# Performance work log

Measured on AMD Instinct MI355X. Metric: run time of the kernel, lower is better.

The kernel has to match this reference:

```python
import jax, jax.numpy as jnp
import numpy as np

D_MODEL = 1024
NUM_HEAD = 16
D_HEAD = 64


def setup_inputs() -> dict:
    key = jax.random.key(0)
    ks = jax.random.split(key, 9)
    b, p = 8, 1024
    s = 1.0 / np.sqrt(D_MODEL)
    inp = {
        "x": jax.random.normal(ks[0], (b, p, D_MODEL), jnp.float32),
        "w_q": jax.random.uniform(ks[1], (D_MODEL, D_MODEL), jnp.float32, -s, s),
        "b_q": jax.random.uniform(ks[2], (D_MODEL,), jnp.float32, -s, s),
        "w_k": jax.random.uniform(ks[3], (D_MODEL, D_MODEL), jnp.float32, -s, s),
        "b_k": jax.random.uniform(ks[4], (D_MODEL,), jnp.float32, -s, s),
        "w_v": jax.random.uniform(ks[5], (D_MODEL, D_MODEL), jnp.float32, -s, s),
        "b_v": jax.random.uniform(ks[6], (D_MODEL,), jnp.float32, -s, s),
        "w_o": jax.random.uniform(ks[7], (D_MODEL, D_MODEL), jnp.float32, -s, s),
        "b_o": jax.random.uniform(ks[8], (D_MODEL,), jnp.float32, -s, s),
    }
    return inp


def reference(x, w_q, b_q, w_k, b_k, w_v, b_v, w_o, b_o):
    b, p, _ = x.shape
    # projections (torch Linear: y = x @ W.T + b; here weights stored [in,out])
    q = x @ w_q + b_q
    k = x @ w_k + b_k
    v = x @ w_v + b_v
    # [b, h, p, d]
    q = q.reshape(b, p, NUM_HEAD, D_HEAD).transpose(0, 2, 1, 3)
    k = k.reshape(b, p, NUM_HEAD, D_HEAD).transpose(0, 2, 1, 3)
    v = v.reshape(b, p, NUM_HEAD, D_HEAD).transpose(0, 2, 1, 3)
    scale = 1.0 / np.sqrt(D_HEAD).astype(np.float32)
    scores = jnp.einsum("bhqd,bhkd->bhqk", q, k) * scale
    attn = jax.nn.softmax(scores, axis=-1)
    out = jnp.einsum("bhqk,bhkd->bhqd", attn, v)
    out = out.transpose(0, 2, 1, 3).reshape(b, p, D_MODEL)
    return out @ w_o + b_o
```

## Files before the change

kernel.cpp:

```cpp
#include <hip/hip_runtime.h>
#include <stdint.h>


typedef __attribute__((ext_vector_type(8))) short short8;
typedef __attribute__((ext_vector_type(4))) short s16x4;
typedef __attribute__((ext_vector_type(4))) float f32x4;

__device__ __forceinline__ short f2bf(float f) {
  unsigned u = __builtin_bit_cast(unsigned, f);
  u += 0x7fffu + ((u >> 16) & 1u);
  return (short)(u >> 16);
}

__device__ __forceinline__ unsigned pk2bf(float a, float b) {
  unsigned ua = __builtin_bit_cast(unsigned, a);
  unsigned ub = __builtin_bit_cast(unsigned, b);
  ua += 0x7fffu + ((ua >> 16) & 1u);
  ub += 0x7fffu + ((ub >> 16) & 1u);
  return (ua >> 16) | (ub & 0xffff0000u);
}

__device__ __forceinline__ unsigned cvtpk(float a, float b) {
  unsigned r;
  asm("v_cvt_pk_bf16_f32 %0, %1, %2" : "=v"(r) : "v"(a), "v"(b));
  return r;
}

__device__ __forceinline__ float fexp2(float x) {
  float r;
  asm("v_exp_f32 %0, %1" : "=v"(r) : "v"(x));
  return r;
}

typedef __attribute__((address_space(3))) void lds_void;
typedef __attribute__((address_space(1))) void gbl_void;
#define GLD16(gp, lp) \
  __builtin_amdgcn_global_load_lds((gbl_void*)(gp), (lds_void*)(lp), 16, 0, 0)

#define MFMA(a, b, c) __builtin_amdgcn_mfma_f32_16x16x32_bf16((a), (b), (c), 0, 0, 0)

__global__ __launch_bounds__(256) void k_prep(const float* __restrict__ x,
                                              short* __restrict__ xb,
                                              const float* __restrict__ s0,
                                              const float* __restrict__ s1,
                                              const float* __restrict__ s2,
                                              const float* __restrict__ s3,
                                              short* __restrict__ d0,
                                              short* __restrict__ d1,
                                              short* __restrict__ d2,
                                              short* __restrict__ d3) {
  if (blockIdx.z == 4) {
    int t = threadIdx.y * 32 + threadIdx.x;
    int bid = blockIdx.y * 32 + blockIdx.x;
#pragma unroll
    for (int j = 0; j < 4; ++j) {
      int i = (bid * 1024 + j * 256 + t) * 8;
      const float4* s = (const float4*)(x + i);
      float4 f0 = s[0], f1 = s[1];
      short8 o;
      o[0] = f2bf(f0.x); o[1] = f2bf(f0.y); o[2] = f2bf(f0.z); o[3] = f2bf(f0.w);
      o[4] = f2bf(f1.x); o[5] = f2bf(f1.y); o[6] = f2bf(f1.z); o[7] = f2bf(f1.w);
      *(short8*)(xb + i) = o;
    }
    return;
  }
  __shared__ float tile[32][33];
  const float* srcs[4] = {s0, s1, s2, s3};
  short* dsts[4] = {d0, d1, d2, d3};
  const float* src = srcs[blockIdx.z];
  short* dst = dsts[blockIdx.z];
  int tx = threadIdx.x, ty = threadIdx.y;
  int x0 = blockIdx.x * 32, y0 = blockIdx.y * 32;
#pragma unroll
  for (int i = 0; i < 32; i += 8)
    tile[ty + i][tx] = src[(y0 + ty + i) * 1024 + x0 + tx];
  __syncthreads();
#pragma unroll
  for (int i = 0; i < 32; i += 8)
    dst[(x0 + ty + i) * 1024 + y0 + tx] = f2bf(tile[tx][ty + i]);
}

__global__ __launch_bounds__(512, 2) void k_gemm_qkv(const short* __restrict__ A,
                                                     const short* __restrict__ Bt,
                                                     const float* __restrict__ bias0,
                                                     const float* __restrict__ bias1,
                                                     const float* __restrict__ bias2,
                                                     short* __restrict__ o0,
                                                     short* __restrict__ o1,
                                                     short* __restrict__ o2) {
  __shared__ __align__(16) short a_lds[4][256 * 32];
  __shared__ __align__(16) short b_lds[4][256 * 32];
  const int tid = threadIdx.x;
  const int l = blockIdx.x;
  const int li = l >> 3;
  const int m0 = ((l & 7) * 4 + (li & 3)) << 8;
  const int n0 = (li >> 2) << 8;

  const int lane = tid & 63;
  const int ll = lane & 15;
  const int qd = lane >> 4;
  const int wm = (tid >> 8) * 128;
  const int wn = ((tid >> 6) & 3) * 64;

  const int srow = tid >> 2;
  const int gc = (tid & 3) ^ ((srow >> 1) & 3);
  const short* ag = A + (long)(m0 + srow) * 1024 + gc * 8;
  const short* bg = Bt + (long)(n0 + srow) * 1024 + gc * 8;

  const int xsl = (qd ^ ((ll >> 1) & 3)) * 8;

  f32x4 acc[8][4] = {};

#define STAGE(t)                                              \
  {                                                           \
    const int _b = (t) & 3;                                   \
    const int _k = (t) * 32;                                  \
    GLD16(ag + _k, &a_lds[_b][tid * 8]);                      \
    GLD16(ag + 131072 + _k, &a_lds[_b][4096 + tid * 8]);      \
    GLD16(bg + _k, &b_lds[_b][tid * 8]);                      \
    GLD16(bg + 131072 + _k, &b_lds[_b][4096 + tid * 8]);      \
  }

#define TILE(kt, VM, PF)                                                     \
  {                                                                          \
    asm volatile("s_waitcnt vmcnt(" #VM ")" ::: "memory");                   \
    __builtin_amdgcn_s_barrier();                                            \
    if (PF) STAGE((kt) + 3);                                                 \
    short8 af[8], bf8[4];                                                    \
    _Pragma("unroll")                                                        \
    for (int mi = 0; mi < 8; ++mi)                                           \
      af[mi] = *(const short8*)&a_lds[(kt) & 3][(wm + mi * 16 + ll) * 32 + xsl]; \
    _Pragma("unroll")                                                        \
    for (int ni = 0; ni < 4; ++ni)                                           \
      bf8[ni] = *(const short8*)&b_lds[(kt) & 3][(wn + ni * 16 + ll) * 32 + xsl]; \
    __builtin_amdgcn_s_setprio(1);                                           \
    _Pragma("unroll")                                                        \
    for (int mi = 0; mi < 8; ++mi)                                           \
      _Pragma("unroll")                                                      \
      for (int ni = 0; ni < 4; ++ni)                                         \
        acc[mi][ni] = MFMA(af[mi], bf8[ni], acc[mi][ni]);                    \
    __builtin_amdgcn_s_setprio(0);                                           \
  }

  STAGE(0); STAGE(1); STAGE(2);

#pragma unroll 4
  for (int kt = 0; kt < 28; ++kt) TILE(kt, 8, 1)
  TILE(28, 8, 1)
  TILE(29, 8, 0)
  TILE(30, 4, 0)
  TILE(31, 0, 0)

#undef TILE
#undef STAGE

  const int which = n0 >> 10;
  const int nb = n0 & 1023;
  if (which == 2) {
    const int b = m0 >> 10;
    const int p0 = (m0 & 1023) + wm;
#pragma unroll
    for (int ni = 0; ni < 4; ++ni) {
      int nl = nb + wn + ni * 16 + ll;
      float bv = bias2[nl];
      int h = nl >> 6, d = nl & 63;
#pragma unroll
      for (int mi = 0; mi < 8; ++mi) {
        int p = p0 + mi * 16 + qd * 4;
        int2 pk;
        pk.x = (int)pk2bf(acc[mi][ni][0] + bv, acc[mi][ni][1] + bv);
        pk.y = (int)pk2bf(acc[mi][ni][2] + bv, acc[mi][ni][3] + bv);
        *(int2*)&o2[(long)(b * 16 + h) * 65536 + d * 1024 + p] = pk;
      }
    }
  } else {
    const float* bias = which ? bias1 : bias0;
    short* o = which ? o1 : o0;
    const float sc = which ? 1.0f : 0.18033688f;
#pragma unroll
    for (int ni = 0; ni < 4; ++ni) {
      int nl = nb + wn + ni * 16 + ll;
      float bv = bias[nl];
      int h = nl >> 6, d = nl & 63;
#pragma unroll
      for (int mi = 0; mi < 8; ++mi)
#pragma unroll
        for (int r = 0; r < 4; ++r) {
          int m = m0 + wm + mi * 16 + qd * 4 + r;
          int b = m >> 10, p = m & 1023;
          o[(long)(b * 16 + h) * 65536 + p * 64 + d] = f2bf((acc[mi][ni][r] + bv) * sc);
        }
    }
  }
}

template <int MODE>
__global__ __launch_bounds__(256, 3) void k_gemm(const short* __restrict__ A,
                                                 const short* __restrict__ Bt,
                                                 const float* __restrict__ bias0,
                                                 const float* __restrict__ bias1,
                                                 const float* __restrict__ bias2,
                                                 short* __restrict__ o0,
                                                 short* __restrict__ o1,
                                                 short* __restrict__ o2,
                                                 float* __restrict__ of) {
  __shared__ __align__(16) short a_lds[128 * 64];
  __shared__ __align__(16) short b_lds[128 * 64];
  const int tid = threadIdx.x;
  const int l = blockIdx.x;
  const int m0 = ((((l & 7) << 3) | ((l >> 3) & 7))) << 7;
  const int n0 = (l >> 6) << 7;
  const int w = tid >> 6;
  const int lane = tid & 63;
  const int ll = lane & 15;
  const int qd = lane >> 4;
  const int wm = (w & 1) * 64;
  const int wn = (w >> 1) * 64;

  const int srow = tid >> 3;
  const int schunk = ((tid & 7) ^ (srow & 7)) * 8;
  const short* ag = A + (long)(m0 + srow) * 1024 + schunk;
  const short* bg = Bt + (long)(n0 + srow) * 1024 + schunk;

  f32x4 acc[4][4] = {};

  for (int kt = 0; kt < 1024; kt += 64) {
#pragma unroll
    for (int j = 0; j < 4; ++j) {
      GLD16(ag + j * 32768 + kt, &a_lds[j * 2048 + tid * 8]);
      GLD16(bg + j * 32768 + kt, &b_lds[j * 2048 + tid * 8]);
    }
    __syncthreads();
#pragma unroll
    for (int kh = 0; kh < 2; ++kh) {
      const int xoff = (((kh * 4 + qd) ^ (ll & 7)) * 8);
      short8 af[4], bfr[4];
#pragma unroll
      for (int mt = 0; mt < 4; ++mt)
        af[mt] = *(const short8*)&a_lds[(wm + mt * 16 + ll) * 64 + xoff];
#pragma unroll
      for (int nt = 0; nt < 4; ++nt)
        bfr[nt] = *(const short8*)&b_lds[(wn + nt * 16 + ll) * 64 + xoff];
#pragma unroll
      for (int mt = 0; mt < 4; ++mt)
#pragma unroll
        for (int nt = 0; nt < 4; ++nt)
          acc[mt][nt] = MFMA(af[mt], bfr[nt], acc[mt][nt]);
    }
    __syncthreads();
  }

  if (MODE == 0) {
  } else {
#pragma unroll
    for (int nt = 0; nt < 4; ++nt) {
      int n = n0 + wn + nt * 16 + ll;
      float bv = bias0[n];
#pragma unroll
      for (int mt = 0; mt < 4; ++mt) {
#pragma unroll
        for (int r = 0; r < 4; ++r) {
          int m = m0 + wm + mt * 16 + qd * 4 + r;
          of[(long)m * 1024 + n] = acc[mt][nt][r] + bv;
        }
      }
    }
  }
}

__global__ __launch_bounds__(256, 4) void k_attn(const short* __restrict__ Q,
                                                 const short* __restrict__ K,
                                                 const short* __restrict__ VT,
                                                 short* __restrict__ O) {
  __shared__ __align__(16) short k_lds[2][4096];
  __shared__ __align__(16) short vt_lds[2][4096];
  const int tid = threadIdx.x;
  const int w = tid >> 6, lane = tid & 63, ll = lane & 15, qd = lane >> 4;
  const int bid = blockIdx.x;
  const int xcd = bid & 7;
  const int inner = bid >> 3;
  const int bh = xcd * 16 + (inner & 15);
  const int qb = inner >> 4;
  const long hoff = (long)bh * 65536;
  const int qr0 = qb * 128 + w * 32;

  const short* qg = Q + hoff + (long)(qr0 + ll) * 64 + qd * 8;
  short8 qf[2][2];
  qf[0][0] = *(const short8*)qg;
  qf[0][1] = *(const short8*)(qg + 32);
  qf[1][0] = *(const short8*)(qg + 1024);
  qf[1][1] = *(const short8*)(qg + 1024 + 32);

  const int sr = tid >> 3;
  const int swz = (tid & 7) ^ (sr & 7);
  const int pr = (sr & 0x23) | ((sr & 0x0C) << 1) | ((sr & 0x10) >> 2);
  const short* kg = K + hoff + pr * 64 + swz * 8;
  const short* vg = VT + hoff + (long)sr * 1024 + swz * 8;

  const int swzr = ll & 7;
  const int fro0 = ll * 64 + ((qd ^ swzr) * 8);
  const int fro1 = ll * 64 + (((4 + qd) ^ swzr) * 8);

  f32x4 oacc[2][4] = {};
  float l_part[2] = {0.f, 0.f};

  GLD16(kg, &k_lds[0][tid * 8]);
  GLD16(kg + 2048, &k_lds[0][2048 + tid * 8]);
  GLD16(vg, &vt_lds[0][tid * 8]);
  GLD16(vg + 32768, &vt_lds[0][2048 + tid * 8]);
  __syncthreads();

#pragma unroll 2
  for (int c = 0; c < 16; ++c) {
    const int cur = c & 1, nxt = cur ^ 1;
    if (c < 15) {
      GLD16(kg + (c + 1) * 4096, &k_lds[nxt][tid * 8]);
      GLD16(kg + (c + 1) * 4096 + 2048, &k_lds[nxt][2048 + tid * 8]);
      GLD16(vg + (c + 1) * 64, &vt_lds[nxt][tid * 8]);
      GLD16(vg + (c + 1) * 64 + 32768, &vt_lds[nxt][2048 + tid * 8]);
    }

    f32x4 s[2][4];
    __builtin_amdgcn_s_setprio(1);
#pragma unroll
    for (int jt = 0; jt < 4; ++jt) {
      short8 kf0 = *(const short8*)&k_lds[cur][jt * 1024 + fro0];
      short8 kf1 = *(const short8*)&k_lds[cur][jt * 1024 + fro1];
      f32x4 t0 = {};
      t0 = MFMA(kf0, qf[0][0], t0);
      t0 = MFMA(kf1, qf[0][1], t0);
      s[0][jt] = t0;
      f32x4 t1 = {};
      t1 = MFMA(kf0, qf[1][0], t1);
      t1 = MFMA(kf1, qf[1][1], t1);
      s[1][jt] = t1;
    }
    __builtin_amdgcn_s_setprio(0);

    short8 pf[2][2];
#pragma unroll
    for (int g = 0; g < 2; ++g) {
      float rs = 0.f;
#pragma unroll
      for (int jt = 0; jt < 4; ++jt)
#pragma unroll
        for (int r = 0; r < 4; ++r) {
          float e = fexp2(s[g][jt][r]);
          s[g][jt][r] = e;
          rs += e;
        }
      l_part[g] += rs;
#pragma unroll
      for (int u = 0; u < 2; ++u) {
        union { short8 v; unsigned x[4]; } pk;
        pk.x[0] = cvtpk(s[g][2 * u][0], s[g][2 * u][1]);
        pk.x[1] = cvtpk(s[g][2 * u][2], s[g][2 * u][3]);
        pk.x[2] = cvtpk(s[g][2 * u + 1][0], s[g][2 * u + 1][1]);
        pk.x[3] = cvtpk(s[g][2 * u + 1][2], s[g][2 * u + 1][3]);
        pf[g][u] = pk.v;
      }
    }

    __builtin_amdgcn_s_setprio(1);
#pragma unroll
    for (int dt = 0; dt < 4; ++dt) {
      short8 vf0 = *(const short8*)&vt_lds[cur][dt * 1024 + fro0];
      short8 vf1 = *(const short8*)&vt_lds[cur][dt * 1024 + fro1];
      oacc[0][dt] = MFMA(vf0, pf[0][0], oacc[0][dt]);
      oacc[0][dt] = MFMA(vf1, pf[0][1], oacc[0][dt]);
      oacc[1][dt] = MFMA(vf0, pf[1][0], oacc[1][dt]);
      oacc[1][dt] = MFMA(vf1, pf[1][1], oacc[1][dt]);
    }
    __builtin_amdgcn_s_setprio(0);
    __syncthreads();
  }

  const int b = bh >> 4, h = bh & 15;
#pragma unroll
  for (int g = 0; g < 2; ++g) {
    float l = l_part[g];
    l += __shfl_xor(l, 16, 64);
    l += __shfl_xor(l, 32, 64);
    const float inv = 1.0f / l;
    const long row = (long)(b * 1024 + qr0 + g * 16 + ll);
#pragma unroll
    for (int dt = 0; dt < 4; ++dt) {
      int2 ov;
      ov.x = (int)cvtpk(oacc[g][dt][0] * inv, oacc[g][dt][1] * inv);
      ov.y = (int)cvtpk(oacc[g][dt][2] * inv, oacc[g][dt][3] * inv);
      *(int2*)&O[row * 1024 + h * 64 + dt * 16 + qd * 4] = ov;
    }
  }
}

extern "C" void kernel_launch(void* const* d_in, const int* in_sizes, int n_in,
                              void* d_out, int out_size, void* d_ws, size_t ws_size,
                              hipStream_t stream) {
  const float* x   = (const float*)d_in[0];
  const float* w_q = (const float*)d_in[1];
  const float* b_q = (const float*)d_in[2];
  const float* w_k = (const float*)d_in[3];
  const float* b_k = (const float*)d_in[4];
  const float* w_v = (const float*)d_in[5];
  const float* b_v = (const float*)d_in[6];
  const float* w_o = (const float*)d_in[7];
  const float* b_o = (const float*)d_in[8];

  char* ws = (char*)d_ws;
  short* xb    = (short*)(ws);
  short* wqkvT = (short*)(ws + (16ull << 20));
  short* woT   = (short*)(ws + (22ull << 20));
  short* qw    = (short*)(ws + (24ull << 20));
  short* kw    = (short*)(ws + (40ull << 20));
  short* vw    = (short*)(ws + (56ull << 20));

  k_prep<<<dim3(32, 32, 5), dim3(32, 8), 0, stream>>>(
      x, xb, w_q, w_k, w_v, w_o,
      wqkvT, wqkvT + (1 << 20), wqkvT + (2 << 20), woT);

  k_gemm_qkv<<<384, 512, 0, stream>>>(xb, wqkvT, b_q, b_k, b_v, qw, kw, vw);

  k_attn<<<dim3(1024), 256, 0, stream>>>(qw, kw, vw, xb);

  k_gemm<1><<<512, 256, 0, stream>>>(xb, woT, b_o, nullptr, nullptr,
                                     nullptr, nullptr, nullptr, (float*)d_out);
}
```

Measured before the change: 241.6 us.

## Interleave QKV GEMM loads with MFMA quarters, MFMA row sums, wider prep tiles

The QKV GEMM now splits each k-tile into four quarters. Each quarter issues one global-to-LDS prefetch and computes a 4x2 MFMA sub-block, with an extra barrier per quarter, and launch bounds are relaxed to one block per CU. The attention kernel now computes softmax row sums with an MFMA against a ones vector, which removes the scalar accumulation and the cross-lane shuffles. The prep kernel processes twice as much data per block and writes packed bf16 pairs, so it launches half as many blocks. The extra barriers and the change in occupancy could add stalls.

```diff
diff --git a/kernel.cpp b/kernel.cpp
--- a/kernel.cpp
+++ b/kernel.cpp
@@ -53,8 +53,8 @@
     int t = threadIdx.y * 32 + threadIdx.x;
     int bid = blockIdx.y * 32 + blockIdx.x;
 #pragma unroll
-    for (int j = 0; j < 4; ++j) {
-      int i = (bid * 1024 + j * 256 + t) * 8;
+    for (int j = 0; j < 8; ++j) {
+      int i = (bid * 2048 + j * 256 + t) * 8;
       const float4* s = (const float4*)(x + i);
       float4 f0 = s[0], f1 = s[1];
       short8 o;
@@ -64,23 +64,26 @@
     }
     return;
   }
-  __shared__ float tile[32][33];
+  __shared__ float tile[64][33];
   const float* srcs[4] = {s0, s1, s2, s3};
   short* dsts[4] = {d0, d1, d2, d3};
   const float* src = srcs[blockIdx.z];
   short* dst = dsts[blockIdx.z];
   int tx = threadIdx.x, ty = threadIdx.y;
-  int x0 = blockIdx.x * 32, y0 = blockIdx.y * 32;
-#pragma unroll
-  for (int i = 0; i < 32; i += 8)
+  int x0 = blockIdx.x * 32, y0 = blockIdx.y * 64;
+#pragma unroll
+  for (int i = 0; i < 64; i += 8)
     tile[ty + i][tx] = src[(y0 + ty + i) * 1024 + x0 + tx];
   __syncthreads();
 #pragma unroll
-  for (int i = 0; i < 32; i += 8)
-    dst[(x0 + ty + i) * 1024 + y0 + tx] = f2bf(tile[tx][ty + i]);
-}
-
-__global__ __launch_bounds__(512, 2) void k_gemm_qkv(const short* __restrict__ A,
+  for (int i = 0; i < 32; i += 8) {
+    int r = ty + i;
+    *(int*)&dst[(x0 + r) * 1024 + y0 + 2 * tx] =
+        (int)pk2bf(tile[2 * tx][r], tile[2 * tx + 1][r]);
+  }
+}
+
+__global__ __launch_bounds__(512, 1) void k_gemm_qkv(const short* __restrict__ A,
                                                      const short* __restrict__ Bt,
                                                      const float* __restrict__ bias0,
                                                      const float* __restrict__ bias1,
@@ -111,38 +114,43 @@
 
   f32x4 acc[8][4] = {};
 
-#define STAGE(t)                                              \
-  {                                                           \
-    const int _b = (t) & 3;                                   \
-    const int _k = (t) * 32;                                  \
-    GLD16(ag + _k, &a_lds[_b][tid * 8]);                      \
-    GLD16(ag + 131072 + _k, &a_lds[_b][4096 + tid * 8]);      \
-    GLD16(bg + _k, &b_lds[_b][tid * 8]);                      \
-    GLD16(bg + 131072 + _k, &b_lds[_b][4096 + tid * 8]);      \
-  }
-
-#define TILE(kt, VM, PF)                                                     \
-  {                                                                          \
-    asm volatile("s_waitcnt vmcnt(" #VM ")" ::: "memory");                   \
-    __builtin_amdgcn_s_barrier();                                            \
-    if (PF) STAGE((kt) + 3);                                                 \
-    short8 af[8], bf8[4];                                                    \
-    _Pragma("unroll")                                                        \
-    for (int mi = 0; mi < 8; ++mi)                                           \
-      af[mi] = *(const short8*)&a_lds[(kt) & 3][(wm + mi * 16 + ll) * 32 + xsl]; \
-    _Pragma("unroll")                                                        \
-    for (int ni = 0; ni < 4; ++ni)                                           \
-      bf8[ni] = *(const short8*)&b_lds[(kt) & 3][(wn + ni * 16 + ll) * 32 + xsl]; \
-    __builtin_amdgcn_s_setprio(1);                                           \
-    _Pragma("unroll")                                                        \
-    for (int mi = 0; mi < 8; ++mi)                                           \
-      _Pragma("unroll")                                                      \
-      for (int ni = 0; ni < 4; ++ni)                                         \
-        acc[mi][ni] = MFMA(af[mi], bf8[ni], acc[mi][ni]);                    \
-    __builtin_amdgcn_s_setprio(0);                                           \
-  }
-
-  STAGE(0); STAGE(1); STAGE(2);
+#define STAGE1(t, q)                                                              \
+  {                                                                               \
+    if ((q) == 0) GLD16(ag + (t) * 32, &a_lds[(t) & 3][tid * 8]);                 \
+    if ((q) == 1) GLD16(ag + 131072 + (t) * 32, &a_lds[(t) & 3][4096 + tid * 8]); \
+    if ((q) == 2) GLD16(bg + (t) * 32, &b_lds[(t) & 3][tid * 8]);                 \
+    if ((q) == 3) GLD16(bg + 131072 + (t) * 32, &b_lds[(t) & 3][4096 + tid * 8]); \
+  }
+
+#define STAGE_ALL(t) { STAGE1(t, 0) STAGE1(t, 1) STAGE1(t, 2) STAGE1(t, 3) }
+
+#define TILE(kt, VM, PF)                                                          \
+  {                                                                               \
+    asm volatile("s_waitcnt vmcnt(" #VM ")" ::: "memory");                        \
+    __builtin_amdgcn_s_barrier();           \
+    _Pragma("unroll")                                                             \
+    for (int q = 0; q < 4; ++q) {                                                 \
+      if (PF) STAGE1((kt) + 3, q);                                                \
+      const int mb = (q >> 1) * 4, nb2 = (q & 1) * 2;                             \
+      short8 af[4], bf2[2];                                                       \
+      _Pragma("unroll")                                                           \
+      for (int i = 0; i < 4; ++i)                                                 \
+        af[i] = *(const short8*)&a_lds[(kt) & 3][(wm + (mb + i) * 16 + ll) * 32 + xsl]; \
+      _Pragma("unroll")                                                           \
+      for (int j = 0; j < 2; ++j)                                                 \
+        bf2[j] = *(const short8*)&b_lds[(kt) & 3][(wn + (nb2 + j) * 16 + ll) * 32 + xsl]; \
+      __builtin_amdgcn_s_barrier();  \
+      __builtin_amdgcn_s_setprio(1);                                              \
+      _Pragma("unroll")                                                           \
+      for (int i = 0; i < 4; ++i)                                                 \
+        _Pragma("unroll")                                                         \
+        for (int j = 0; j < 2; ++j)                                               \
+          acc[mb + i][nb2 + j] = MFMA(af[i], bf2[j], acc[mb + i][nb2 + j]);       \
+      __builtin_amdgcn_s_setprio(0);                                              \
+    }                                                                             \
+  }
+
+  STAGE_ALL(0); STAGE_ALL(1); STAGE_ALL(2);
 
 #pragma unroll 4
   for (int kt = 0; kt < 28; ++kt) TILE(kt, 8, 1)
@@ -152,7 +160,8 @@
   TILE(31, 0, 0)
 
 #undef TILE
-#undef STAGE
+#undef STAGE_ALL
+#undef STAGE1
 
   const int which = n0 >> 10;
   const int nb = n0 & 1023;
@@ -250,8 +259,7 @@
     __syncthreads();
   }
 
-  if (MODE == 0) {
-  } else {
+  if (MODE == 1) {
 #pragma unroll
     for (int nt = 0; nt < 4; ++nt) {
       int n = n0 + wn + nt * 16 + ll;
@@ -301,8 +309,12 @@
   const int fro0 = ll * 64 + ((qd ^ swzr) * 8);
   const int fro1 = ll * 64 + (((4 + qd) ^ swzr) * 8);
 
+  short8 ones;
+#pragma unroll
+  for (int i = 0; i < 8; ++i) ones[i] = (short)0x3F80;
+
   f32x4 oacc[2][4] = {};
-  float l_part[2] = {0.f, 0.f};
+  f32x4 lacc[2] = {};
 
   GLD16(kg, &k_lds[0][tid * 8]);
   GLD16(kg + 2048, &k_lds[0][2048 + tid * 8]);
@@ -340,16 +352,11 @@
     short8 pf[2][2];
 #pragma unroll
     for (int g = 0; g < 2; ++g) {
-      float rs = 0.f;
 #pragma unroll
       for (int jt = 0; jt < 4; ++jt)
 #pragma unroll
-        for (int r = 0; r < 4; ++r) {
-          float e = fexp2(s[g][jt][r]);
-          s[g][jt][r] = e;
-          rs += e;
-        }
-      l_part[g] += rs;
+        for (int r = 0; r < 4; ++r)
+          s[g][jt][r] = fexp2(s[g][jt][r]);
 #pragma unroll
       for (int u = 0; u < 2; ++u) {
         union { short8 v; unsigned x[4]; } pk;
@@ -371,6 +378,10 @@
       oacc[1][dt] = MFMA(vf0, pf[1][0], oacc[1][dt]);
       oacc[1][dt] = MFMA(vf1, pf[1][1], oacc[1][dt]);
     }
+    lacc[0] = MFMA(ones, pf[0][0], lacc[0]);
+    lacc[0] = MFMA(ones, pf[0][1], lacc[0]);
+    lacc[1] = MFMA(ones, pf[1][0], lacc[1]);
+    lacc[1] = MFMA(ones, pf[1][1], lacc[1]);
     __builtin_amdgcn_s_setprio(0);
     __syncthreads();
   }
@@ -378,10 +389,7 @@
   const int b = bh >> 4, h = bh & 15;
 #pragma unroll
   for (int g = 0; g < 2; ++g) {
-    float l = l_part[g];
-    l += __shfl_xor(l, 16, 64);
-    l += __shfl_xor(l, 32, 64);
-    const float inv = 1.0f / l;
+    const float inv = 1.0f / lacc[g][0];
     const long row = (long)(b * 1024 + qr0 + g * 16 + ll);
 #pragma unroll
     for (int dt = 0; dt < 4; ++dt) {
@@ -414,7 +422,7 @@
   short* kw    = (short*)(ws + (40ull << 20));
   short* vw    = (short*)(ws + (56ull << 20));
 
-  k_prep<<<dim3(32, 32, 5), dim3(32, 8), 0, stream>>>(
+  k_prep<<<dim3(32, 16, 5), dim3(32, 8), 0, stream>>>(
       x, xb, w_q, w_k, w_v, w_o,
       wqkvT, wqkvT + (1 << 20), wqkvT + (2 << 20), woT);
 
```

New measurement: 244.1 us. Within noise of the previous version (+1.0%).
